# Optimization experiments

Measured on AMD Instinct MI355X. Metric: run time of the kernel, lower is better.

## Reference

```python
import jax, jax.numpy as jnp
import numpy as np

B, N, DIN = 32, 4096, 256
K, D, H = 8, 256, 512
ITERS = 3
EPS = 1e-8
LN_EPS = 1e-5
SCALE = D ** -0.5


def _ln(x, g, b):
    m = jnp.mean(x, axis=-1, keepdims=True)
    v = jnp.var(x, axis=-1, keepdims=True)
    return (x - m) * jax.lax.rsqrt(v + LN_EPS) * g + b


def setup_inputs() -> dict:
    key = jax.random.key(0)
    ks = jax.random.split(key, 12)
    lin = lambda k, o, i: jax.random.uniform(k, (o, i), jnp.float32, -1.0, 1.0) * (i ** -0.5)
    return {
        "x": jax.random.normal(ks[0], (B, N, DIN), jnp.float32),
        "noise": jax.random.normal(ks[1], (B, K, D), jnp.float32),
        "nx_g": jnp.ones((DIN,), jnp.float32), "nx_b": jnp.zeros((DIN,), jnp.float32),
        "ns_g": jnp.ones((D,), jnp.float32), "ns_b": jnp.zeros((D,), jnp.float32),
        "mu": jax.random.normal(ks[2], (1, 1, D), jnp.float32) * 0.02,
        "logsigma": jnp.zeros((1, 1, D), jnp.float32),
        "Wq": lin(ks[3], D, D), "Wk": lin(ks[4], D, DIN), "Wv": lin(ks[5], D, DIN),
        "W_ih": lin(ks[6], 3 * D, D), "W_hh": lin(ks[7], 3 * D, D),
        "b_ih": jnp.zeros((3 * D,), jnp.float32), "b_hh": jnp.zeros((3 * D,), jnp.float32),
        "mlp_g": jnp.ones((D,), jnp.float32), "mlp_b": jnp.zeros((D,), jnp.float32),
        "W1": lin(ks[8], H, D), "b1": jnp.zeros((H,), jnp.float32),
        "W2": lin(ks[9], D, H), "b2": jnp.zeros((D,), jnp.float32),
    }


def _gru(u, h, W_ih, W_hh, b_ih, b_hh):
    # PyTorch GRUCell: gates ordered (r, z, n)
    gi = u @ W_ih.T + b_ih   # [BK, 3D]
    gh = h @ W_hh.T + b_hh
    ir, iz, inn = jnp.split(gi, 3, axis=-1)
    hr, hz, hn = jnp.split(gh, 3, axis=-1)
    r = jax.nn.sigmoid(ir + hr)
    z = jax.nn.sigmoid(iz + hz)
    n = jnp.tanh(inn + r * hn)
    return (1.0 - z) * n + z * h


def reference(x, noise, nx_g, nx_b, ns_g, ns_b, mu, logsigma, Wq, Wk, Wv,
              W_ih, W_hh, b_ih, b_hh, mlp_g, mlp_b, W1, b1, W2, b2):
    xn = _ln(x, nx_g, nx_b)                       # [B,N,DIN]
    k = xn @ Wk.T                                 # [B,N,D]
    v = xn @ Wv.T                                 # [B,N,D]
    slots = mu + jnp.exp(logsigma) * noise        # [B,K,D]
    attn = None
    for _ in range(ITERS):
        s = _ln(slots, ns_g, ns_b)
        q = s @ Wq.T                              # [B,K,D]
        logits = jnp.einsum('bkd,bnd->bkn', q, k) * SCALE
        attn = jax.nn.softmax(logits, axis=1) + EPS   # softmax over slots
        attn = attn / jnp.sum(attn, axis=1, keepdims=True)
        updates = jnp.einsum('bkn,bnd->bkd', attn, v)
        h = _gru(updates.reshape(B * K, D), slots.reshape(B * K, D),
                 W_ih, W_hh, b_ih, b_hh).reshape(B, K, D)
        m = _ln(h, mlp_g, mlp_b)
        m = jax.nn.gelu(m @ W1.T + b1, approximate=False) @ W2.T + b2
        slots = h + m
    return slots, attn
```

## Files before the change

### kernel.cpp

```cpp
#include <hip/hip_runtime.h>
#include <hip/hip_bf16.h>
#include <math.h>

#define LN_EPS 1e-5f
#define EPSA 1e-8f
#define SCALE 0.0625f

typedef __attribute__((ext_vector_type(8))) short short8;
typedef __attribute__((ext_vector_type(4))) short short4_t;
typedef __attribute__((ext_vector_type(4))) float f32x4;

__device__ inline unsigned short f2bf(float f) {
    union { float f; unsigned int u; } v; v.f = f;
    unsigned int r = v.u + 0x7fffu + ((v.u >> 16) & 1u);
    return (unsigned short)(r >> 16);
}
__device__ inline float bf2f(unsigned short h) {
    union { unsigned int u; float f; } v; v.u = ((unsigned int)h) << 16;
    return v.f;
}
__device__ inline float sigmoidf_(float x) { return 1.0f / (1.0f + expf(-x)); }

__global__ __launch_bounds__(256) void pack_wb(const float* __restrict__ Wk,
                                               const float* __restrict__ Wv,
                                               __hip_bfloat16* __restrict__ Wcb) {
    int idx = blockIdx.x * 256 + threadIdx.x;
    int n = idx >> 8, k = idx & 255;
    float v = (n < 256) ? Wk[n*256 + k] : Wv[(n-256)*256 + k];
    Wcb[idx] = __float2bfloat16(v);
}

__global__ __launch_bounds__(256) void gemm_kv_fused(const float* __restrict__ x,
                                                     const float* __restrict__ nx_g,
                                                     const float* __restrict__ nx_b,
                                                     const __hip_bfloat16* __restrict__ Wcb,
                                                     __hip_bfloat16* __restrict__ kp,
                                                     __hip_bfloat16* __restrict__ vp) {
    __shared__ short As[64*256];
    __shared__ float gb[512];
    const int t = threadIdx.x;
    const int row0 = blockIdx.x * 64;
    const int r = t >> 2, q = t & 3;

    float4 xr[16];
    const float* xrow = x + (size_t)(row0 + r) * 256 + q*4;
    #pragma unroll
    for (int j = 0; j < 16; ++j) xr[j] = *(const float4*)(xrow + j*16);
    gb[t] = nx_g[t]; gb[t+256] = nx_b[t];

    float s = 0.f, s2 = 0.f;
    #pragma unroll
    for (int j = 0; j < 16; ++j) {
        s  += xr[j].x + xr[j].y + xr[j].z + xr[j].w;
        s2 += xr[j].x*xr[j].x + xr[j].y*xr[j].y + xr[j].z*xr[j].z + xr[j].w*xr[j].w;
    }
    s  += __shfl_xor(s, 1);  s2 += __shfl_xor(s2, 1);
    s  += __shfl_xor(s, 2);  s2 += __shfl_xor(s2, 2);
    float m = s * (1.0f/256.0f);
    float var = s2 * (1.0f/256.0f) - m*m;
    float rstd = rsqrtf(var + LN_EPS);
    __syncthreads();

    #pragma unroll
    for (int j = 0; j < 16; ++j) {
        int c = q*4 + j*16;
        float4 g = *(const float4*)&gb[c];
        float4 bb = *(const float4*)&gb[256 + c];
        short4_t o;
        o[0] = (short)f2bf((xr[j].x - m)*rstd*g.x + bb.x);
        o[1] = (short)f2bf((xr[j].y - m)*rstd*g.y + bb.y);
        o[2] = (short)f2bf((xr[j].z - m)*rstd*g.z + bb.z);
        o[3] = (short)f2bf((xr[j].w - m)*rstd*g.w + bb.w);
        int byte = ((r << 9) + (c << 1)) ^ ((r & 7) << 4);
        *(short4_t*)((char*)As + byte) = o;
    }
    __syncthreads();

    const int l = t & 63, w = t >> 6;
    const int lr = l & 15, lk = l >> 4;
    const int arow = w*16 + lr;
    short8 af[8];
    #pragma unroll
    for (int ks = 0; ks < 8; ++ks) {
        int lin = (arow << 9) + (lk << 4) + (ks << 6);
        af[ks] = *(short8*)((char*)As + (lin ^ ((arow & 7) << 4)));
    }
    for (int c = 0; c < 8; ++c) {
        f32x4 acc[4];
        #pragma unroll
        for (int bf = 0; bf < 4; ++bf) acc[bf] = (f32x4){0.f,0.f,0.f,0.f};
        #pragma unroll
        for (int ks = 0; ks < 8; ++ks) {
            #pragma unroll
            for (int bf = 0; bf < 4; ++bf) {
                const short8 bv = *(const short8*)((const short*)Wcb +
                    ((size_t)(c*64 + bf*16 + lr))*256 + ks*32 + lk*8);
                acc[bf] = __builtin_amdgcn_mfma_f32_16x16x32_bf16(af[ks], bv, acc[bf], 0, 0, 0);
            }
        }
        __hip_bfloat16* dst = (c < 4) ? kp : vp;
        const int cb = c*64 - ((c >= 4) ? 256 : 0);
        #pragma unroll
        for (int bf = 0; bf < 4; ++bf) {
            int col = cb + bf*16 + lr;
            #pragma unroll
            for (int jj = 0; jj < 4; ++jj) {
                int row = row0 + w*16 + lk*4 + jj;
                dst[(size_t)row*256 + col] = __float2bfloat16(acc[bf][jj]);
            }
        }
    }
}

__global__ __launch_bounds__(256) void slots_init(const float* __restrict__ noise,
                                                  const float* __restrict__ mu,
                                                  const float* __restrict__ logsigma,
                                                  float* __restrict__ slots) {
    int i = blockIdx.x * 256 + threadIdx.x;
    int d = i & 255;
    slots[i] = mu[d] + expf(logsigma[d]) * noise[i];
}

__global__ __launch_bounds__(256) void qproj(const float* __restrict__ slots,
                                             const float* __restrict__ ns_g,
                                             const float* __restrict__ ns_b,
                                             const float* __restrict__ Wq,
                                             unsigned short* __restrict__ qb) {
    int row = blockIdx.x, t = threadIdx.x;
    int b = row >> 3, s8 = row & 7;
    __shared__ float sn[256];
    __shared__ float red[8];
    float v = slots[row*256 + t];
    float s = v, s2 = v*v;
    for (int off = 32; off > 0; off >>= 1) {
        s  += __shfl_down(s, off);
        s2 += __shfl_down(s2, off);
    }
    if ((t & 63) == 0) { red[t>>6] = s; red[4 + (t>>6)] = s2; }
    __syncthreads();
    float S  = red[0]+red[1]+red[2]+red[3];
    float S2 = red[4]+red[5]+red[6]+red[7];
    float m = S * (1.0f/256.0f);
    float var = S2 * (1.0f/256.0f) - m*m;
    float rs = rsqrtf(var + LN_EPS);
    sn[t] = (v - m) * rs * ns_g[t] + ns_b[t];
    __syncthreads();
    float acc = 0.0f;
    const float4* wrow = (const float4*)(Wq + t*256);
    #pragma unroll 8
    for (int i = 0; i < 64; ++i) {
        float4 w = wrow[i];
        acc += w.x*sn[4*i] + w.y*sn[4*i+1] + w.z*sn[4*i+2] + w.w*sn[4*i+3];
    }
    unsigned short hh = f2bf(acc);
    unsigned short ll = f2bf(acc - bf2f(hh));
    qb[((size_t)(b*16 + s8))*256 + t]     = hh;
    qb[((size_t)(b*16 + 8 + s8))*256 + t] = ll;
}

__global__ __launch_bounds__(256) void attn_fused(const __hip_bfloat16* __restrict__ kp,
                                                  const __hip_bfloat16* __restrict__ vp,
                                                  const unsigned short* __restrict__ qb,
                                                  float* __restrict__ attn_out,
                                                  float* __restrict__ partial) {
    __shared__ short as_[16*264];
    __shared__ float asf[8*256];
    const int b = blockIdx.x >> 4, c = blockIdx.x & 15;
    const int t = threadIdx.x, l = t & 63, w = t >> 6;
    const int lr = l & 15, lk = l >> 4;
    const int n0 = c * 256;

    short8 qf[8];
    #pragma unroll
    for (int ks = 0; ks < 8; ++ks)
        qf[ks] = *(const short8*)(qb + ((size_t)(b*16 + lr))*256 + ks*32 + lk*8);

    f32x4 acc[4];
    #pragma unroll
    for (int nf = 0; nf < 4; ++nf) acc[nf] = (f32x4){0.f,0.f,0.f,0.f};
    #pragma unroll
    for (int ks = 0; ks < 8; ++ks) {
        #pragma unroll
        for (int nf = 0; nf < 4; ++nf) {
            const short8 a = *(const short8*)((const short*)kp +
                ((size_t)(b*4096 + n0 + w*64 + nf*16 + lr))*256 + ks*32 + lk*8);
            acc[nf] = __builtin_amdgcn_mfma_f32_16x16x32_bf16(a, qf[ks], acc[nf], 0, 0, 0);
        }
    }

    const float renorm = 1.0f / (1.0f + 8.0f*EPSA);
    #pragma unroll
    for (int nf = 0; nf < 4; ++nf) {
        #pragma unroll
        for (int jj = 0; jj < 4; ++jj) {
            float lg = acc[nf][jj];
            lg += __shfl_xor(lg, 8);
            lg *= SCALE;
            float mx = lg;
            mx = fmaxf(mx, __shfl_xor(mx, 1));
            mx = fmaxf(mx, __shfl_xor(mx, 2));
            mx = fmaxf(mx, __shfl_xor(mx, 4));
            float e = expf(lg - mx);
            float ss = e;
            ss += __shfl_xor(ss, 1);
            ss += __shfl_xor(ss, 2);
            ss += __shfl_xor(ss, 4);
            acc[nf][jj] = (e / ss + EPSA) * renorm;
        }
    }

    if (lr < 8) {
        #pragma unroll
        for (int nf = 0; nf < 4; ++nf) {
            int nl = w*64 + nf*16 + lk*4;
            float4 fa = {acc[nf][0], acc[nf][1], acc[nf][2], acc[nf][3]};
            *(float4*)&asf[lr*256 + nl] = fa;
            short4_t ah, al;
            #pragma unroll
            for (int jj = 0; jj < 4; ++jj) {
                unsigned short h = f2bf(acc[nf][jj]);
                ah[jj] = (short)h;
                al[jj] = (short)f2bf(acc[nf][jj] - bf2f(h));
            }
            *(short4_t*)&as_[lr*264 + nl]       = ah;
            *(short4_t*)&as_[(8 + lr)*264 + nl] = al;
        }
    }
    __syncthreads();

    {
        int slot = t >> 5, nn = (t & 31) * 8;
        float4 f0 = *(float4*)&asf[slot*256 + nn];
        float4 f1 = *(float4*)&asf[slot*256 + nn + 4];
        float* dstp = attn_out + ((size_t)(b*8 + slot))*4096 + n0 + nn;
        *(float4*)dstp = f0;
        *(float4*)(dstp + 4) = f1;
    }

    f32x4 pacc[4];
    #pragma unroll
    for (int df = 0; df < 4; ++df) pacc[df] = (f32x4){0.f,0.f,0.f,0.f};
    #pragma unroll
    for (int ks = 0; ks < 8; ++ks) {
        const short8 a = *(const short8*)&as_[lr*264 + ks*32 + lk*8];
        #pragma unroll
        for (int df = 0; df < 4; ++df) {
            short8 bv;
            #pragma unroll
            for (int j = 0; j < 8; ++j)
                bv[j] = ((const short*)vp)[((size_t)(b*4096 + n0 + ks*32 + lk*8 + j))*256
                                           + w*64 + df*16 + lr];
            pacc[df] = __builtin_amdgcn_mfma_f32_16x16x32_bf16(a, bv, pacc[df], 0, 0, 0);
        }
    }
    #pragma unroll
    for (int df = 0; df < 4; ++df) {
        #pragma unroll
        for (int jj = 0; jj < 4; ++jj) {
            float v = pacc[df][jj];
            float vo = __shfl_xor(v, 32);
            if (l < 32) {
                int slot = lk*4 + jj;
                partial[((size_t)((b*16 + c)*8 + slot))*256 + w*64 + df*16 + lr] = v + vo;
            }
        }
    }
}

__global__ __launch_bounds__(256) void gru_mlp(const float* __restrict__ partial,
                                               const float* __restrict__ slots,
                                               const float* __restrict__ W_ih,
                                               const float* __restrict__ W_hh,
                                               const float* __restrict__ b_ih,
                                               const float* __restrict__ b_hh,
                                               const float* __restrict__ mlp_g,
                                               const float* __restrict__ mlp_b,
                                               const float* __restrict__ W1,
                                               const float* __restrict__ b1,
                                               const float* __restrict__ W2,
                                               const float* __restrict__ b2,
                                               float* __restrict__ slots_out,
                                               float* __restrict__ out_slots,
                                               int last) {
    int rrow = blockIdx.x, t = threadIdx.x;
    int b = rrow >> 3, k = rrow & 7;
    __shared__ float u_s[256], h_s[256];
    __shared__ float hn[256], m1[512];
    __shared__ float red[8];
    float u = 0.0f;
    #pragma unroll
    for (int ch = 0; ch < 16; ++ch)
        u += partial[(((size_t)(b*16 + ch)*8 + k)*256) + t];
    u_s[t] = u;
    h_s[t] = slots[rrow*256 + t];
    __syncthreads();

    float gi_r = b_ih[t], gi_z = b_ih[256 + t], gi_n = b_ih[512 + t];
    float gh_r = b_hh[t], gh_z = b_hh[256 + t], gh_n = b_hh[512 + t];
    const float4* wir = (const float4*)(W_ih + (size_t)t*256);
    const float4* wiz = (const float4*)(W_ih + (size_t)(256 + t)*256);
    const float4* win = (const float4*)(W_ih + (size_t)(512 + t)*256);
    const float4* whr = (const float4*)(W_hh + (size_t)t*256);
    const float4* whz = (const float4*)(W_hh + (size_t)(256 + t)*256);
    const float4* whn = (const float4*)(W_hh + (size_t)(512 + t)*256);
    #pragma unroll 4
    for (int i = 0; i < 64; ++i) {
        float u0 = u_s[4*i], u1 = u_s[4*i+1], u2 = u_s[4*i+2], u3 = u_s[4*i+3];
        float h0 = h_s[4*i], h1 = h_s[4*i+1], h2 = h_s[4*i+2], h3 = h_s[4*i+3];
        float4 wv;
        wv = wir[i]; gi_r += wv.x*u0 + wv.y*u1 + wv.z*u2 + wv.w*u3;
        wv = wiz[i]; gi_z += wv.x*u0 + wv.y*u1 + wv.z*u2 + wv.w*u3;
        wv = win[i]; gi_n += wv.x*u0 + wv.y*u1 + wv.z*u2 + wv.w*u3;
        wv = whr[i]; gh_r += wv.x*h0 + wv.y*h1 + wv.z*h2 + wv.w*h3;
        wv = whz[i]; gh_z += wv.x*h0 + wv.y*h1 + wv.z*h2 + wv.w*h3;
        wv = whn[i]; gh_n += wv.x*h0 + wv.y*h1 + wv.z*h2 + wv.w*h3;
    }
    float rg = sigmoidf_(gi_r + gh_r);
    float zg = sigmoidf_(gi_z + gh_z);
    float ng = tanhf(gi_n + rg * gh_n);
    float hval = (1.0f - zg)*ng + zg*h_s[t];

    float s = hval, s2 = hval*hval;
    for (int off = 32; off > 0; off >>= 1) {
        s  += __shfl_down(s, off);
        s2 += __shfl_down(s2, off);
    }
    __syncthreads();
    if ((t & 63) == 0) { red[t>>6] = s; red[4 + (t>>6)] = s2; }
    __syncthreads();
    float S  = red[0]+red[1]+red[2]+red[3];
    float S2 = red[4]+red[5]+red[6]+red[7];
    float m = S * (1.0f/256.0f);
    float var = S2 * (1.0f/256.0f) - m*m;
    float rs = rsqrtf(var + LN_EPS);
    hn[t] = (hval - m) * rs * mlp_g[t] + mlp_b[t];
    __syncthreads();

    #pragma unroll
    for (int jj = 0; jj < 2; ++jj) {
        int j = t + jj*256;
        float acc = b1[j];
        const float4* wv = (const float4*)(W1 + (size_t)j*256);
        #pragma unroll 8
        for (int i = 0; i < 64; ++i) {
            float4 ww = wv[i];
            acc += ww.x*hn[4*i] + ww.y*hn[4*i+1] + ww.z*hn[4*i+2] + ww.w*hn[4*i+3];
        }
        m1[j] = 0.5f * acc * (1.0f + erff(acc * 0.70710678118654752f));
    }
    __syncthreads();

    float acc = b2[t];
    const float4* w2 = (const float4*)(W2 + (size_t)t*512);
    #pragma unroll 8
    for (int i = 0; i < 128; ++i) {
        float4 ww = w2[i];
        acc += ww.x*m1[4*i] + ww.y*m1[4*i+1] + ww.z*m1[4*i+2] + ww.w*m1[4*i+3];
    }
    float res = hval + acc;
    slots_out[rrow*256 + t] = res;
    if (last) out_slots[rrow*256 + t] = res;
}

extern "C" void kernel_launch(void* const* d_in, const int* in_sizes, int n_in,
                              void* d_out, int out_size, void* d_ws, size_t ws_size,
                              hipStream_t stream) {
    const float* x        = (const float*)d_in[0];
    const float* noise    = (const float*)d_in[1];
    const float* nx_g     = (const float*)d_in[2];
    const float* nx_b     = (const float*)d_in[3];
    const float* ns_g     = (const float*)d_in[4];
    const float* ns_b     = (const float*)d_in[5];
    const float* mu       = (const float*)d_in[6];
    const float* logsigma = (const float*)d_in[7];
    const float* Wq       = (const float*)d_in[8];
    const float* Wk       = (const float*)d_in[9];
    const float* Wv       = (const float*)d_in[10];
    const float* W_ih     = (const float*)d_in[11];
    const float* W_hh     = (const float*)d_in[12];
    const float* b_ih     = (const float*)d_in[13];
    const float* b_hh     = (const float*)d_in[14];
    const float* mlp_g    = (const float*)d_in[15];
    const float* mlp_b    = (const float*)d_in[16];
    const float* W1       = (const float*)d_in[17];
    const float* b1       = (const float*)d_in[18];
    const float* W2       = (const float*)d_in[19];
    const float* b2       = (const float*)d_in[20];

    float* out_slots = (float*)d_out;
    float* out_attn  = (float*)d_out + 65536;

    char* ws = (char*)d_ws;
    __hip_bfloat16* Wcb = (__hip_bfloat16*)ws;
    unsigned short* qb  = (unsigned short*)(Wcb + 131072);
    __hip_bfloat16* kp  = (__hip_bfloat16*)(qb + 131072);
    __hip_bfloat16* vp  = kp + (size_t)33554432;
    float* slots  = (float*)(vp + (size_t)33554432);
    float* partial= slots + 65536;

    pack_wb<<<512, 256, 0, stream>>>(Wk, Wv, Wcb);
    gemm_kv_fused<<<2048, 256, 0, stream>>>(x, nx_g, nx_b, Wcb, kp, vp);
    slots_init<<<256, 256, 0, stream>>>(noise, mu, logsigma, slots);

    for (int it = 0; it < 3; ++it) {
        qproj<<<256, 256, 0, stream>>>(slots, ns_g, ns_b, Wq, qb);
        attn_fused<<<512, 256, 0, stream>>>(kp, vp, qb, out_attn, partial);
        gru_mlp<<<256, 256, 0, stream>>>(partial, slots, W_ih, W_hh, b_ih, b_hh,
                                         mlp_g, mlp_b, W1, b1, W2, b2,
                                         slots, out_slots, it == 2);
    }
}
```

Baseline: 836.1 us.

## Fold Wk into query and Wv after attention, skip K/V materialization

Removes the large K/V projection GEMM and its bf16 K/V buffers. The query is multiplied by Wq·Wk, precomputed once into a fused matrix, so logits come straight from the layer-normed x. The attention-weighted sum is taken over normalized x, and Wv is applied afterwards on only 8 slots per batch. Each iteration now re-reads and re-normalizes x (about 128MB in fp32) and splits it into hi/lo bf16 parts, instead of reading 64MB of bf16 K/V. Weight matrices are also transposed once so the GRU/MLP kernel gets coalesced loads and reuses each weight across 4 slot rows.

```diff
diff --git a/kernel.cpp b/kernel.cpp
--- a/kernel.cpp
+++ b/kernel.cpp
@@ -7,7 +7,6 @@
 #define SCALE 0.0625f
 
 typedef __attribute__((ext_vector_type(8))) short short8;
-typedef __attribute__((ext_vector_type(4))) short short4_t;
 typedef __attribute__((ext_vector_type(4))) float f32x4;
 
 __device__ inline unsigned short f2bf(float f) {
@@ -21,94 +20,62 @@
 }
 __device__ inline float sigmoidf_(float x) { return 1.0f / (1.0f + expf(-x)); }
 
-__global__ __launch_bounds__(256) void pack_wb(const float* __restrict__ Wk,
-                                               const float* __restrict__ Wv,
-                                               __hip_bfloat16* __restrict__ Wcb) {
-    int idx = blockIdx.x * 256 + threadIdx.x;
-    int n = idx >> 8, k = idx & 255;
-    float v = (n < 256) ? Wk[n*256 + k] : Wv[(n-256)*256 + k];
-    Wcb[idx] = __float2bfloat16(v);
-}
-
-__global__ __launch_bounds__(256) void gemm_kv_fused(const float* __restrict__ x,
-                                                     const float* __restrict__ nx_g,
-                                                     const float* __restrict__ nx_b,
-                                                     const __hip_bfloat16* __restrict__ Wcb,
-                                                     __hip_bfloat16* __restrict__ kp,
-                                                     __hip_bfloat16* __restrict__ vp) {
-    __shared__ short As[64*256];
-    __shared__ float gb[512];
+__global__ __launch_bounds__(256) void wqk_prep(const float* __restrict__ Wq,
+                                                const float* __restrict__ Wk,
+                                                float* __restrict__ Wqk) {
+    __shared__ float wq[256][8];
     const int t = threadIdx.x;
-    const int row0 = blockIdx.x * 64;
-    const int r = t >> 2, q = t & 3;
-
-    float4 xr[16];
-    const float* xrow = x + (size_t)(row0 + r) * 256 + q*4;
-    #pragma unroll
-    for (int j = 0; j < 16; ++j) xr[j] = *(const float4*)(xrow + j*16);
-    gb[t] = nx_g[t]; gb[t+256] = nx_b[t];
-
-    float s = 0.f, s2 = 0.f;
-    #pragma unroll
-    for (int j = 0; j < 16; ++j) {
-        s  += xr[j].x + xr[j].y + xr[j].z + xr[j].w;
-        s2 += xr[j].x*xr[j].x + xr[j].y*xr[j].y + xr[j].z*xr[j].z + xr[j].w*xr[j].w;
-    }
-    s  += __shfl_xor(s, 1);  s2 += __shfl_xor(s2, 1);
-    s  += __shfl_xor(s, 2);  s2 += __shfl_xor(s2, 2);
-    float m = s * (1.0f/256.0f);
-    float var = s2 * (1.0f/256.0f) - m*m;
-    float rstd = rsqrtf(var + LN_EPS);
-    __syncthreads();
-
-    #pragma unroll
-    for (int j = 0; j < 16; ++j) {
-        int c = q*4 + j*16;
-        float4 g = *(const float4*)&gb[c];
-        float4 bb = *(const float4*)&gb[256 + c];
-        short4_t o;
-        o[0] = (short)f2bf((xr[j].x - m)*rstd*g.x + bb.x);
-        o[1] = (short)f2bf((xr[j].y - m)*rstd*g.y + bb.y);
-        o[2] = (short)f2bf((xr[j].z - m)*rstd*g.z + bb.z);
-        o[3] = (short)f2bf((xr[j].w - m)*rstd*g.w + bb.w);
-        int byte = ((r << 9) + (c << 1)) ^ ((r & 7) << 4);
-        *(short4_t*)((char*)As + byte) = o;
-    }
-    __syncthreads();
-
-    const int l = t & 63, w = t >> 6;
-    const int lr = l & 15, lk = l >> 4;
-    const int arow = w*16 + lr;
-    short8 af[8];
-    #pragma unroll
-    for (int ks = 0; ks < 8; ++ks) {
-        int lin = (arow << 9) + (lk << 4) + (ks << 6);
-        af[ks] = *(short8*)((char*)As + (lin ^ ((arow & 7) << 4)));
-    }
-    for (int c = 0; c < 8; ++c) {
-        f32x4 acc[4];
-        #pragma unroll
-        for (int bf = 0; bf < 4; ++bf) acc[bf] = (f32x4){0.f,0.f,0.f,0.f};
-        #pragma unroll
-        for (int ks = 0; ks < 8; ++ks) {
-            #pragma unroll
-            for (int bf = 0; bf < 4; ++bf) {
-                const short8 bv = *(const short8*)((const short*)Wcb +
-                    ((size_t)(c*64 + bf*16 + lr))*256 + ks*32 + lk*8);
-                acc[bf] = __builtin_amdgcn_mfma_f32_16x16x32_bf16(af[ks], bv, acc[bf], 0, 0, 0);
-            }
-        }
-        __hip_bfloat16* dst = (c < 4) ? kp : vp;
-        const int cb = c*64 - ((c >= 4) ? 256 : 0);
-        #pragma unroll
-        for (int bf = 0; bf < 4; ++bf) {
-            int col = cb + bf*16 + lr;
-            #pragma unroll
-            for (int jj = 0; jj < 4; ++jj) {
-                int row = row0 + w*16 + lk*4 + jj;
-                dst[(size_t)row*256 + col] = __float2bfloat16(acc[bf][jj]);
-            }
-        }
+    const int d0 = blockIdx.x * 8;
+    float4 a = *(const float4*)(Wq + (size_t)t*256 + d0);
+    float4 b = *(const float4*)(Wq + (size_t)t*256 + d0 + 4);
+    wq[t][0]=a.x; wq[t][1]=a.y; wq[t][2]=a.z; wq[t][3]=a.w;
+    wq[t][4]=b.x; wq[t][5]=b.y; wq[t][6]=b.z; wq[t][7]=b.w;
+    __syncthreads();
+    float acc[8] = {0,0,0,0,0,0,0,0};
+    for (int i = 0; i < 256; ++i) {
+        float wk = Wk[(size_t)i*256 + t];
+        #pragma unroll
+        for (int j = 0; j < 8; ++j) acc[j] += wq[i][j] * wk;
+    }
+    #pragma unroll
+    for (int j = 0; j < 8; ++j) Wqk[(size_t)(d0 + j)*256 + t] = acc[j];
+}
+
+__global__ __launch_bounds__(256) void wtrans(const float* __restrict__ Wv,
+                                              const float* __restrict__ W_ih,
+                                              const float* __restrict__ W_hh,
+                                              const float* __restrict__ W1,
+                                              const float* __restrict__ W2,
+                                              float* __restrict__ WvT,
+                                              float* __restrict__ WihT,
+                                              float* __restrict__ WhhT,
+                                              float* __restrict__ W1T,
+                                              float* __restrict__ W2T) {
+    __shared__ float tile[64][65];
+    const int t = threadIdx.x;
+    int id = blockIdx.x;
+    const float* in; float* out; int O, K, base;
+    if      (id < 16)  { in = Wv;   out = WvT;  O = 256; K = 256; base = 0;   }
+    else if (id < 64)  { in = W_ih; out = WihT; O = 768; K = 256; base = 16;  }
+    else if (id < 112) { in = W_hh; out = WhhT; O = 768; K = 256; base = 64;  }
+    else if (id < 144) { in = W1;   out = W1T;  O = 512; K = 256; base = 112; }
+    else               { in = W2;   out = W2T;  O = 256; K = 512; base = 144; }
+    int local = id - base;
+    int tiles_o = O >> 6;
+    int o0 = (local % tiles_o) * 64;
+    int k0 = (local / tiles_o) * 64;
+    #pragma unroll
+    for (int jj = 0; jj < 16; ++jj) {
+        int flat = jj*256 + t;
+        int i = flat >> 6, j = flat & 63;
+        tile[i][j] = in[(size_t)(o0 + i)*K + k0 + j];
+    }
+    __syncthreads();
+    #pragma unroll
+    for (int jj = 0; jj < 16; ++jj) {
+        int flat = jj*256 + t;
+        int jp = flat >> 6, ip = flat & 63;
+        out[(size_t)(k0 + jp)*O + o0 + ip] = tile[ip][jp];
     }
 }
 
@@ -121,245 +88,354 @@
     slots[i] = mu[d] + expf(logsigma[d]) * noise[i];
 }
 
-__global__ __launch_bounds__(256) void qproj(const float* __restrict__ slots,
-                                             const float* __restrict__ ns_g,
-                                             const float* __restrict__ ns_b,
-                                             const float* __restrict__ Wq,
-                                             unsigned short* __restrict__ qb) {
-    int row = blockIdx.x, t = threadIdx.x;
-    int b = row >> 3, s8 = row & 7;
-    __shared__ float sn[256];
-    __shared__ float red[8];
-    float v = slots[row*256 + t];
-    float s = v, s2 = v*v;
-    for (int off = 32; off > 0; off >>= 1) {
-        s  += __shfl_down(s, off);
-        s2 += __shfl_down(s2, off);
-    }
-    if ((t & 63) == 0) { red[t>>6] = s; red[4 + (t>>6)] = s2; }
-    __syncthreads();
-    float S  = red[0]+red[1]+red[2]+red[3];
-    float S2 = red[4]+red[5]+red[6]+red[7];
-    float m = S * (1.0f/256.0f);
-    float var = S2 * (1.0f/256.0f) - m*m;
-    float rs = rsqrtf(var + LN_EPS);
-    sn[t] = (v - m) * rs * ns_g[t] + ns_b[t];
-    __syncthreads();
-    float acc = 0.0f;
-    const float4* wrow = (const float4*)(Wq + t*256);
-    #pragma unroll 8
-    for (int i = 0; i < 64; ++i) {
-        float4 w = wrow[i];
-        acc += w.x*sn[4*i] + w.y*sn[4*i+1] + w.z*sn[4*i+2] + w.w*sn[4*i+3];
-    }
-    unsigned short hh = f2bf(acc);
-    unsigned short ll = f2bf(acc - bf2f(hh));
-    qb[((size_t)(b*16 + s8))*256 + t]     = hh;
-    qb[((size_t)(b*16 + 8 + s8))*256 + t] = ll;
-}
-
-__global__ __launch_bounds__(256) void attn_fused(const __hip_bfloat16* __restrict__ kp,
-                                                  const __hip_bfloat16* __restrict__ vp,
-                                                  const unsigned short* __restrict__ qb,
+__global__ __launch_bounds__(256) void qkproj(const float* __restrict__ slots,
+                                              const float* __restrict__ ns_g,
+                                              const float* __restrict__ ns_b,
+                                              const float* __restrict__ Wqk,
+                                              unsigned short* __restrict__ qkb) {
+    __shared__ float sl[8][256];
+    const int b = blockIdx.x, t = threadIdx.x;
+    #pragma unroll
+    for (int s = 0; s < 8; ++s)
+        sl[s][t] = slots[((size_t)(b*8 + s))*256 + t];
+    __syncthreads();
+    const int m = t >> 5, c = t & 31;
+    float v[8];
+    float s1 = 0.f, s2 = 0.f;
+    #pragma unroll
+    for (int j = 0; j < 8; ++j) {
+        v[j] = sl[m][c + 32*j];
+        s1 += v[j]; s2 += v[j]*v[j];
+    }
+    s1 += __shfl_xor(s1, 1);  s2 += __shfl_xor(s2, 1);
+    s1 += __shfl_xor(s1, 2);  s2 += __shfl_xor(s2, 2);
+    s1 += __shfl_xor(s1, 4);  s2 += __shfl_xor(s2, 4);
+    s1 += __shfl_xor(s1, 8);  s2 += __shfl_xor(s2, 8);
+    s1 += __shfl_xor(s1, 16); s2 += __shfl_xor(s2, 16);
+    float mean = s1 * (1.0f/256.0f);
+    float var  = s2 * (1.0f/256.0f) - mean*mean;
+    float rstd = rsqrtf(var + LN_EPS);
+    #pragma unroll
+    for (int j = 0; j < 8; ++j) {
+        int col = c + 32*j;
+        sl[m][col] = (v[j] - mean) * rstd * ns_g[col] + ns_b[col];
+    }
+    __syncthreads();
+    float acc[8] = {0,0,0,0,0,0,0,0};
+    for (int d = 0; d < 256; ++d) {
+        float w = Wqk[(size_t)d*256 + t];
+        #pragma unroll
+        for (int s = 0; s < 8; ++s) acc[s] += sl[s][d] * w;
+    }
+    #pragma unroll
+    for (int s = 0; s < 8; ++s) {
+        unsigned short hh = f2bf(acc[s]);
+        unsigned short ll = f2bf(acc[s] - bf2f(hh));
+        qkb[((size_t)(b*16 + s))*256 + t]     = hh;
+        qkb[((size_t)(b*16 + 8 + s))*256 + t] = ll;
+    }
+}
+
+__global__ __launch_bounds__(256) void attn_fused(const float* __restrict__ x,
+                                                  const float* __restrict__ nx_g,
+                                                  const float* __restrict__ nx_b,
+                                                  const unsigned short* __restrict__ qkb,
                                                   float* __restrict__ attn_out,
                                                   float* __restrict__ partial) {
-    __shared__ short as_[16*264];
-    __shared__ float asf[8*256];
+    __shared__ unsigned short xh[32*264];
+    __shared__ unsigned short xl[32*264];
+    __shared__ float xf[32*257];
+    __shared__ float lgP[2*32*8];
+    __shared__ float asf[8*32];
     const int b = blockIdx.x >> 4, c = blockIdx.x & 15;
     const int t = threadIdx.x, l = t & 63, w = t >> 6;
     const int lr = l & 15, lk = l >> 4;
-    const int n0 = c * 256;
+    const int tile = w & 1, part = w >> 1;
+    const int m = t >> 5;
+    const int dcol = (t & 31) * 8;
+    const size_t xbase = ((size_t)b*4096 + (size_t)c*256) * 256;
+
+    float4 g0 = *(const float4*)(nx_g + dcol);
+    float4 g1 = *(const float4*)(nx_g + dcol + 4);
+    float4 bb0 = *(const float4*)(nx_b + dcol);
+    float4 bb1 = *(const float4*)(nx_b + dcol + 4);
 
     short8 qf[8];
     #pragma unroll
     for (int ks = 0; ks < 8; ++ks)
-        qf[ks] = *(const short8*)(qb + ((size_t)(b*16 + lr))*256 + ks*32 + lk*8);
-
-    f32x4 acc[4];
-    #pragma unroll
-    for (int nf = 0; nf < 4; ++nf) acc[nf] = (f32x4){0.f,0.f,0.f,0.f};
-    #pragma unroll
-    for (int ks = 0; ks < 8; ++ks) {
-        #pragma unroll
-        for (int nf = 0; nf < 4; ++nf) {
-            const short8 a = *(const short8*)((const short*)kp +
-                ((size_t)(b*4096 + n0 + w*64 + nf*16 + lr))*256 + ks*32 + lk*8);
-            acc[nf] = __builtin_amdgcn_mfma_f32_16x16x32_bf16(a, qf[ks], acc[nf], 0, 0, 0);
-        }
-    }
+        qf[ks] = *(const short8*)(qkb + ((size_t)(b*16 + lr))*256 + ks*32 + lk*8);
+
+    float4 sx[4][2];
+
+    float pacc[8] = {0,0,0,0,0,0,0,0};
+    const int axs = t >> 5;
+
+    #define STAGE_LOAD(CH) {                                              \
+        _Pragma("unroll")                                                 \
+        for (int j = 0; j < 4; ++j) {                                     \
+            int row = m + 8*j;                                            \
+            const float* src = x + xbase + (size_t)((CH)*32 + row)*256 + dcol; \
+            sx[j][0] = *(const float4*)src;                               \
+            sx[j][1] = *(const float4*)(src + 4);                         \
+        } }
+
+    #define STAGE_WRITE() {                                               \
+        _Pragma("unroll")                                                 \
+        for (int j = 0; j < 4; ++j) {                                     \
+            float e[8] = { sx[j][0].x, sx[j][0].y, sx[j][0].z, sx[j][0].w,\
+                           sx[j][1].x, sx[j][1].y, sx[j][1].z, sx[j][1].w };\
+            float s1 = 0.f, s2 = 0.f;                                     \
+            _Pragma("unroll")                                             \
+            for (int q = 0; q < 8; ++q) { s1 += e[q]; s2 += e[q]*e[q]; }  \
+            s1 += __shfl_xor(s1, 1);  s2 += __shfl_xor(s2, 1);            \
+            s1 += __shfl_xor(s1, 2);  s2 += __shfl_xor(s2, 2);            \
+            s1 += __shfl_xor(s1, 4);  s2 += __shfl_xor(s2, 4);            \
+            s1 += __shfl_xor(s1, 8);  s2 += __shfl_xor(s2, 8);            \
+            s1 += __shfl_xor(s1, 16); s2 += __shfl_xor(s2, 16);           \
+            float mean = s1 * (1.0f/256.0f);                              \
+            float var  = s2 * (1.0f/256.0f) - mean*mean;                  \
+            float rstd = rsqrtf(var + LN_EPS);                            \
+            e[0] = (e[0]-mean)*rstd*g0.x + bb0.x;                         \
+            e[1] = (e[1]-mean)*rstd*g0.y + bb0.y;                         \
+            e[2] = (e[2]-mean)*rstd*g0.z + bb0.z;                         \
+            e[3] = (e[3]-mean)*rstd*g0.w + bb0.w;                         \
+            e[4] = (e[4]-mean)*rstd*g1.x + bb1.x;                         \
+            e[5] = (e[5]-mean)*rstd*g1.y + bb1.y;                         \
+            e[6] = (e[6]-mean)*rstd*g1.z + bb1.z;                         \
+            e[7] = (e[7]-mean)*rstd*g1.w + bb1.w;                         \
+            int row = m + 8*j;                                            \
+            short8 hh, ll;                                                \
+            _Pragma("unroll")                                             \
+            for (int q = 0; q < 8; ++q) {                                 \
+                unsigned short hv = f2bf(e[q]);                           \
+                hh[q] = (short)hv;                                        \
+                ll[q] = (short)f2bf(e[q] - bf2f(hv));                     \
+            }                                                             \
+            *(short8*)((char*)xh + (size_t)row*528 + (size_t)dcol*2) = hh;\
+            *(short8*)((char*)xl + (size_t)row*528 + (size_t)dcol*2) = ll;\
+            *(float4*)(xf + row*257 + dcol)     = (float4){e[0],e[1],e[2],e[3]};\
+            *(float4*)(xf + row*257 + dcol + 4) = (float4){e[4],e[5],e[6],e[7]};\
+        } }
+
+    STAGE_LOAD(0);
+    STAGE_WRITE();
+    __syncthreads();
 
     const float renorm = 1.0f / (1.0f + 8.0f*EPSA);
-    #pragma unroll
-    for (int nf = 0; nf < 4; ++nf) {
-        #pragma unroll
-        for (int jj = 0; jj < 4; ++jj) {
-            float lg = acc[nf][jj];
-            lg += __shfl_xor(lg, 8);
-            lg *= SCALE;
-            float mx = lg;
-            mx = fmaxf(mx, __shfl_xor(mx, 1));
-            mx = fmaxf(mx, __shfl_xor(mx, 2));
-            mx = fmaxf(mx, __shfl_xor(mx, 4));
-            float e = expf(lg - mx);
-            float ss = e;
-            ss += __shfl_xor(ss, 1);
-            ss += __shfl_xor(ss, 2);
-            ss += __shfl_xor(ss, 4);
-            acc[nf][jj] = (e / ss + EPSA) * renorm;
-        }
-    }
-
-    if (lr < 8) {
-        #pragma unroll
-        for (int nf = 0; nf < 4; ++nf) {
-            int nl = w*64 + nf*16 + lk*4;
-            float4 fa = {acc[nf][0], acc[nf][1], acc[nf][2], acc[nf][3]};
-            *(float4*)&asf[lr*256 + nl] = fa;
-            short4_t ah, al;
+    for (int chunk = 0; chunk < 8; ++chunk) {
+        if (chunk < 7) STAGE_LOAD(chunk + 1);
+
+        {
+            const unsigned short* xa = part ? xl : xh;
+            f32x4 acc = (f32x4){0.f,0.f,0.f,0.f};
+            #pragma unroll
+            for (int ks = 0; ks < 8; ++ks) {
+                short8 a = *(const short8*)((const char*)xa +
+                    (size_t)(tile*16 + lr)*528 + (size_t)(ks*32 + lk*8)*2);
+                acc = __builtin_amdgcn_mfma_f32_16x16x32_bf16(a, qf[ks], acc, 0, 0, 0);
+            }
             #pragma unroll
             for (int jj = 0; jj < 4; ++jj) {
-                unsigned short h = f2bf(acc[nf][jj]);
-                ah[jj] = (short)h;
-                al[jj] = (short)f2bf(acc[nf][jj] - bf2f(h));
-            }
-            *(short4_t*)&as_[lr*264 + nl]       = ah;
-            *(short4_t*)&as_[(8 + lr)*264 + nl] = al;
-        }
-    }
-    __syncthreads();
-
-    {
-        int slot = t >> 5, nn = (t & 31) * 8;
-        float4 f0 = *(float4*)&asf[slot*256 + nn];
-        float4 f1 = *(float4*)&asf[slot*256 + nn + 4];
-        float* dstp = attn_out + ((size_t)(b*8 + slot))*4096 + n0 + nn;
-        *(float4*)dstp = f0;
-        *(float4*)(dstp + 4) = f1;
-    }
-
-    f32x4 pacc[4];
-    #pragma unroll
-    for (int df = 0; df < 4; ++df) pacc[df] = (f32x4){0.f,0.f,0.f,0.f};
-    #pragma unroll
-    for (int ks = 0; ks < 8; ++ks) {
-        const short8 a = *(const short8*)&as_[lr*264 + ks*32 + lk*8];
-        #pragma unroll
-        for (int df = 0; df < 4; ++df) {
-            short8 bv;
-            #pragma unroll
-            for (int j = 0; j < 8; ++j)
-                bv[j] = ((const short*)vp)[((size_t)(b*4096 + n0 + ks*32 + lk*8 + j))*256
-                                           + w*64 + df*16 + lr];
-            pacc[df] = __builtin_amdgcn_mfma_f32_16x16x32_bf16(a, bv, pacc[df], 0, 0, 0);
-        }
-    }
-    #pragma unroll
-    for (int df = 0; df < 4; ++df) {
-        #pragma unroll
-        for (int jj = 0; jj < 4; ++jj) {
-            float v = pacc[df][jj];
-            float vo = __shfl_xor(v, 32);
-            if (l < 32) {
-                int slot = lk*4 + jj;
-                partial[((size_t)((b*16 + c)*8 + slot))*256 + w*64 + df*16 + lr] = v + vo;
-            }
-        }
-    }
+                float v = acc[jj];
+                v += __shfl_xor(v, 8);
+                if (!(l & 8))
+                    lgP[part*256 + (tile*16 + (l>>4)*4 + jj)*8 + (l & 7)] = v;
+            }
+        }
+        __syncthreads();
+
+        if (t < 32) {
+            int n = t;
+            float lg[8], mx = -1e30f;
+            #pragma unroll
+            for (int s = 0; s < 8; ++s) {
+                lg[s] = (lgP[n*8 + s] + lgP[256 + n*8 + s]) * SCALE;
+                mx = fmaxf(mx, lg[s]);
+            }
+            float ssum = 0.f;
+            #pragma unroll
+            for (int s = 0; s < 8; ++s) { lg[s] = expf(lg[s] - mx); ssum += lg[s]; }
+            float inv = 1.0f / ssum;
+            #pragma unroll
+            for (int s = 0; s < 8; ++s)
+                asf[s*32 + n] = (lg[s]*inv + EPSA) * renorm;
+        }
+        __syncthreads();
+
+        {
+            int s = t >> 5, n = t & 31;
+            attn_out[((size_t)(b*8 + s))*4096 + c*256 + chunk*32 + n] = asf[s*32 + n];
+        }
+        {
+            const float* arow = &asf[axs*32];
+            #pragma unroll 4
+            for (int n = 0; n < 32; ++n) {
+                float a = arow[n];
+                float4 v0 = *(const float4*)(xf + n*257 + dcol);
+                float4 v1 = *(const float4*)(xf + n*257 + dcol + 4);
+                pacc[0] += a*v0.x; pacc[1] += a*v0.y; pacc[2] += a*v0.z; pacc[3] += a*v0.w;
+                pacc[4] += a*v1.x; pacc[5] += a*v1.y; pacc[6] += a*v1.z; pacc[7] += a*v1.w;
+            }
+        }
+        __syncthreads();
+
+        if (chunk < 7) {
+            STAGE_WRITE();
+            __syncthreads();
+        }
+    }
+
+    float* p = partial + (((size_t)(b*16 + c)*8 + axs))*256 + dcol;
+    *(float4*)p       = (float4){pacc[0], pacc[1], pacc[2], pacc[3]};
+    *(float4*)(p + 4) = (float4){pacc[4], pacc[5], pacc[6], pacc[7]};
+    #undef STAGE_LOAD
+    #undef STAGE_WRITE
 }
 
 __global__ __launch_bounds__(256) void gru_mlp(const float* __restrict__ partial,
                                                const float* __restrict__ slots,
-                                               const float* __restrict__ W_ih,
-                                               const float* __restrict__ W_hh,
+                                               const float* __restrict__ WvT,
+                                               const float* __restrict__ WihT,
+                                               const float* __restrict__ WhhT,
                                                const float* __restrict__ b_ih,
                                                const float* __restrict__ b_hh,
                                                const float* __restrict__ mlp_g,
                                                const float* __restrict__ mlp_b,
-                                               const float* __restrict__ W1,
+                                               const float* __restrict__ W1T,
                                                const float* __restrict__ b1,
-                                               const float* __restrict__ W2,
+                                               const float* __restrict__ W2T,
                                                const float* __restrict__ b2,
                                                float* __restrict__ slots_out,
                                                float* __restrict__ out_slots,
                                                int last) {
-    int rrow = blockIdx.x, t = threadIdx.x;
-    int b = rrow >> 3, k = rrow & 7;
-    __shared__ float u_s[256], h_s[256];
-    __shared__ float hn[256], m1[512];
-    __shared__ float red[8];
-    float u = 0.0f;
-    #pragma unroll
-    for (int ch = 0; ch < 16; ++ch)
-        u += partial[(((size_t)(b*16 + ch)*8 + k)*256) + t];
-    u_s[t] = u;
-    h_s[t] = slots[rrow*256 + t];
-    __syncthreads();
-
-    float gi_r = b_ih[t], gi_z = b_ih[256 + t], gi_n = b_ih[512 + t];
-    float gh_r = b_hh[t], gh_z = b_hh[256 + t], gh_n = b_hh[512 + t];
-    const float4* wir = (const float4*)(W_ih + (size_t)t*256);
-    const float4* wiz = (const float4*)(W_ih + (size_t)(256 + t)*256);
-    const float4* win = (const float4*)(W_ih + (size_t)(512 + t)*256);
-    const float4* whr = (const float4*)(W_hh + (size_t)t*256);
-    const float4* whz = (const float4*)(W_hh + (size_t)(256 + t)*256);
-    const float4* whn = (const float4*)(W_hh + (size_t)(512 + t)*256);
-    #pragma unroll 4
-    for (int i = 0; i < 64; ++i) {
-        float u0 = u_s[4*i], u1 = u_s[4*i+1], u2 = u_s[4*i+2], u3 = u_s[4*i+3];
-        float h0 = h_s[4*i], h1 = h_s[4*i+1], h2 = h_s[4*i+2], h3 = h_s[4*i+3];
-        float4 wv;
-        wv = wir[i]; gi_r += wv.x*u0 + wv.y*u1 + wv.z*u2 + wv.w*u3;
-        wv = wiz[i]; gi_z += wv.x*u0 + wv.y*u1 + wv.z*u2 + wv.w*u3;
-        wv = win[i]; gi_n += wv.x*u0 + wv.y*u1 + wv.z*u2 + wv.w*u3;
-        wv = whr[i]; gh_r += wv.x*h0 + wv.y*h1 + wv.z*h2 + wv.w*h3;
-        wv = whz[i]; gh_z += wv.x*h0 + wv.y*h1 + wv.z*h2 + wv.w*h3;
-        wv = whn[i]; gh_n += wv.x*h0 + wv.y*h1 + wv.z*h2 + wv.w*h3;
-    }
-    float rg = sigmoidf_(gi_r + gh_r);
-    float zg = sigmoidf_(gi_z + gh_z);
-    float ng = tanhf(gi_n + rg * gh_n);
-    float hval = (1.0f - zg)*ng + zg*h_s[t];
-
-    float s = hval, s2 = hval*hval;
-    for (int off = 32; off > 0; off >>= 1) {
-        s  += __shfl_down(s, off);
-        s2 += __shfl_down(s2, off);
-    }
-    __syncthreads();
-    if ((t & 63) == 0) { red[t>>6] = s; red[4 + (t>>6)] = s2; }
-    __syncthreads();
-    float S  = red[0]+red[1]+red[2]+red[3];
-    float S2 = red[4]+red[5]+red[6]+red[7];
-    float m = S * (1.0f/256.0f);
-    float var = S2 * (1.0f/256.0f) - m*m;
-    float rs = rsqrtf(var + LN_EPS);
-    hn[t] = (hval - m) * rs * mlp_g[t] + mlp_b[t];
-    __syncthreads();
-
-    #pragma unroll
-    for (int jj = 0; jj < 2; ++jj) {
-        int j = t + jj*256;
-        float acc = b1[j];
-        const float4* wv = (const float4*)(W1 + (size_t)j*256);
-        #pragma unroll 8
-        for (int i = 0; i < 64; ++i) {
-            float4 ww = wv[i];
-            acc += ww.x*hn[4*i] + ww.y*hn[4*i+1] + ww.z*hn[4*i+2] + ww.w*hn[4*i+3];
-        }
-        m1[j] = 0.5f * acc * (1.0f + erff(acc * 0.70710678118654752f));
-    }
-    __syncthreads();
-
-    float acc = b2[t];
-    const float4* w2 = (const float4*)(W2 + (size_t)t*512);
-    #pragma unroll 8
-    for (int i = 0; i < 128; ++i) {
-        float4 ww = w2[i];
-        acc += ww.x*m1[4*i] + ww.y*m1[4*i+1] + ww.z*m1[4*i+2] + ww.w*m1[4*i+3];
-    }
-    float res = hval + acc;
-    slots_out[rrow*256 + t] = res;
-    if (last) out_slots[rrow*256 + t] = res;
+    __shared__ float ax_s[4][256], u_s[4][256], h_s[4][256];
+    __shared__ float hn[4][256], m1s[4][512];
+    __shared__ float redS[4][4], redS2[4][4];
+    const int t = threadIdx.x, l = t & 63, w = t >> 6;
+    const int r0 = blockIdx.x * 4;
+    const int b = r0 >> 3;
+
+    #pragma unroll
+    for (int i = 0; i < 4; ++i) {
+        int k = (r0 + i) & 7;
+        float a = 0.f;
+        #pragma unroll
+        for (int ch = 0; ch < 16; ++ch)
+            a += partial[(((size_t)(b*16 + ch)*8 + k))*256 + t];
+        ax_s[i][t] = a;
+        h_s[i][t] = slots[(size_t)(r0 + i)*256 + t];
+    }
+    __syncthreads();
+
+    {
+        float acc[4] = {0,0,0,0};
+        for (int d = 0; d < 256; ++d) {
+            float wv = WvT[(size_t)d*256 + t];
+            #pragma unroll
+            for (int i = 0; i < 4; ++i) acc[i] += ax_s[i][d] * wv;
+        }
+        #pragma unroll
+        for (int i = 0; i < 4; ++i) u_s[i][t] = acc[i];
+    }
+    __syncthreads();
+
+    float hval[4];
+    {
+        float air[4] = {0,0,0,0}, aiz[4] = {0,0,0,0}, ain[4] = {0,0,0,0};
+        float ahr[4] = {0,0,0,0}, ahz[4] = {0,0,0,0}, ahn[4] = {0,0,0,0};
+        for (int d = 0; d < 256; ++d) {
+            float wir = WihT[(size_t)d*768 + t];
+            float wiz = WihT[(size_t)d*768 + 256 + t];
+            float win = WihT[(size_t)d*768 + 512 + t];
+            float whr = WhhT[(size_t)d*768 + t];
+            float whz = WhhT[(size_t)d*768 + 256 + t];
+            float whn = WhhT[(size_t)d*768 + 512 + t];
+            #pragma unroll
+            for (int i = 0; i < 4; ++i) {
+                float u = u_s[i][d], h = h_s[i][d];
+                air[i] += u*wir; aiz[i] += u*wiz; ain[i] += u*win;
+                ahr[i] += h*whr; ahz[i] += h*whz; ahn[i] += h*whn;
+            }
+        }
+        float bir = b_ih[t], biz = b_ih[256 + t], bin = b_ih[512 + t];
+        float bhr = b_hh[t], bhz = b_hh[256 + t], bhn = b_hh[512 + t];
+        #pragma unroll
+        for (int i = 0; i < 4; ++i) {
+            float rg = sigmoidf_(air[i] + bir + ahr[i] + bhr);
+            float zg = sigmoidf_(aiz[i] + biz + ahz[i] + bhz);
+            float ng = tanhf(ain[i] + bin + rg * (ahn[i] + bhn));
+            hval[i] = (1.0f - zg)*ng + zg*h_s[i][t];
+        }
+    }
+
+    {
+        float s1[4], s2[4];
+        #pragma unroll
+        for (int i = 0; i < 4; ++i) { s1[i] = hval[i]; s2[i] = hval[i]*hval[i]; }
+        #pragma unroll
+        for (int off = 1; off < 64; off <<= 1) {
+            #pragma unroll
+            for (int i = 0; i < 4; ++i) {
+                s1[i] += __shfl_xor(s1[i], off);
+                s2[i] += __shfl_xor(s2[i], off);
+            }
+        }
+        if (l == 0) {
+            #pragma unroll
+            for (int i = 0; i < 4; ++i) { redS[w][i] = s1[i]; redS2[w][i] = s2[i]; }
+        }
+        __syncthreads();
+        #pragma unroll
+        for (int i = 0; i < 4; ++i) {
+            float S  = redS[0][i] + redS[1][i] + redS[2][i] + redS[3][i];
+            float S2 = redS2[0][i] + redS2[1][i] + redS2[2][i] + redS2[3][i];
+            float mean = S * (1.0f/256.0f);
+            float var  = S2 * (1.0f/256.0f) - mean*mean;
+            float rstd = rsqrtf(var + LN_EPS);
+            hn[i][t] = (hval[i] - mean) * rstd * mlp_g[t] + mlp_b[t];
+        }
+    }
+    __syncthreads();
+
+    {
+        float acc0[4], acc1[4];
+        float bb0 = b1[t], bb1 = b1[256 + t];
+        #pragma unroll
+        for (int i = 0; i < 4; ++i) { acc0[i] = bb0; acc1[i] = bb1; }
+        for (int d = 0; d < 256; ++d) {
+            float wa = W1T[(size_t)d*512 + t];
+            float wb = W1T[(size_t)d*512 + 256 + t];
+            #pragma unroll
+            for (int i = 0; i < 4; ++i) {
+                float h = hn[i][d];
+                acc0[i] += h*wa; acc1[i] += h*wb;
+            }
+        }
+        #pragma unroll
+        for (int i = 0; i < 4; ++i) {
+            m1s[i][t]       = 0.5f*acc0[i]*(1.0f + erff(acc0[i]*0.70710678118654752f));
+            m1s[i][t + 256] = 0.5f*acc1[i]*(1.0f + erff(acc1[i]*0.70710678118654752f));
+        }
+    }
+    __syncthreads();
+
+    {
+        float acc[4];
+        float bb = b2[t];
+        #pragma unroll
+        for (int i = 0; i < 4; ++i) acc[i] = bb;
+        for (int d = 0; d < 512; ++d) {
+            float w2 = W2T[(size_t)d*256 + t];
+            #pragma unroll
+            for (int i = 0; i < 4; ++i) acc[i] += m1s[i][d] * w2;
+        }
+        #pragma unroll
+        for (int i = 0; i < 4; ++i) {
+            float res = hval[i] + acc[i];
+            slots_out[(size_t)(r0 + i)*256 + t] = res;
+            if (last) out_slots[(size_t)(r0 + i)*256 + t] = res;
+        }
+    }
 }
 
 extern "C" void kernel_launch(void* const* d_in, const int* in_sizes, int n_in,
@@ -390,23 +466,26 @@
     float* out_slots = (float*)d_out;
     float* out_attn  = (float*)d_out + 65536;
 
-    char* ws = (char*)d_ws;
-    __hip_bfloat16* Wcb = (__hip_bfloat16*)ws;
-    unsigned short* qb  = (unsigned short*)(Wcb + 131072);
-    __hip_bfloat16* kp  = (__hip_bfloat16*)(qb + 131072);
-    __hip_bfloat16* vp  = kp + (size_t)33554432;
-    float* slots  = (float*)(vp + (size_t)33554432);
-    float* partial= slots + 65536;
-
-    pack_wb<<<512, 256, 0, stream>>>(Wk, Wv, Wcb);
-    gemm_kv_fused<<<2048, 256, 0, stream>>>(x, nx_g, nx_b, Wcb, kp, vp);
+    float* ws = (float*)d_ws;
+    float* Wqk   = ws;
+    float* WvT   = Wqk   + 65536;
+    float* WihT  = WvT   + 65536;
+    float* WhhT  = WihT  + 196608;
+    float* W1T   = WhhT  + 196608;
+    float* W2T   = W1T   + 131072;
+    unsigned short* qkb = (unsigned short*)(W2T + 131072);
+    float* slots   = (float*)(qkb + 131072);
+    float* partial = slots + 65536;
+
+    wqk_prep<<<32, 256, 0, stream>>>(Wq, Wk, Wqk);
+    wtrans<<<176, 256, 0, stream>>>(Wv, W_ih, W_hh, W1, W2, WvT, WihT, WhhT, W1T, W2T);
     slots_init<<<256, 256, 0, stream>>>(noise, mu, logsigma, slots);
 
     for (int it = 0; it < 3; ++it) {
-        qproj<<<256, 256, 0, stream>>>(slots, ns_g, ns_b, Wq, qb);
-        attn_fused<<<512, 256, 0, stream>>>(kp, vp, qb, out_attn, partial);
-        gru_mlp<<<256, 256, 0, stream>>>(partial, slots, W_ih, W_hh, b_ih, b_hh,
-                                         mlp_g, mlp_b, W1, b1, W2, b2,
-                                         slots, out_slots, it == 2);
-    }
-}
+        qkproj<<<32, 256, 0, stream>>>(slots, ns_g, ns_b, Wqk, qkb);
+        attn_fused<<<512, 256, 0, stream>>>(x, nx_g, nx_b, qkb, out_attn, partial);
+        gru_mlp<<<64, 256, 0, stream>>>(partial, slots, WvT, WihT, WhhT, b_ih, b_hh,
+                                        mlp_g, mlp_b, W1T, b1, W2T, b2,
+                                        slots, out_slots, it == 2);
+    }
+}
```

Measured after the change: 847.4 us. No clear change (+1.4%).
